# Optimization experiments

Measured on AMD Instinct MI355X. Metric: run time of the kernel, lower is better.

## Reference

```python
import jax, jax.numpy as jnp
from jax import lax
import numpy as np

T_LOW, T_HIGH = 100.0, 200.0  # module defaults
H_IMG, W_IMG = 2048, 2048


def setup_inputs() -> dict:
    key = jax.random.key(0)
    x = jax.random.uniform(key, (H_IMG, W_IMG), dtype=jnp.float32)  # image in [0,1]
    return {"x": x}


def _sh(p, dy, dx, H, W):
    # shifted view of a 1-pixel-padded array
    return p[1 + dy:1 + dy + H, 1 + dx:1 + dx + W]


def _canny(x):
    H, W = x.shape
    # (x*255).astype(uint8): quantize (floor), values assumed in [0,1]
    img = jnp.clip(jnp.floor(x * 255.0), 0.0, 255.0)

    # --- 3x3 Sobel gradients, replicate border (cv2 default) ---
    p = jnp.pad(img, 1, mode='edge')
    s = lambda dy, dx: _sh(p, dy, dx, H, W)
    gx = (s(-1, 1) + 2.0 * s(0, 1) + s(1, 1)) - (s(-1, -1) + 2.0 * s(0, -1) + s(1, -1))
    gy = (s(1, -1) + 2.0 * s(1, 0) + s(1, 1)) - (s(-1, -1) + 2.0 * s(-1, 0) + s(-1, 1))
    mag = jnp.abs(gx) + jnp.abs(gy)  # L1 gradient magnitude (cv2 L2gradient=False)

    # --- non-maximum suppression along quantized gradient direction ---
    ang = jnp.mod(jnp.degrees(jnp.arctan2(gy, gx)), 180.0)
    mp = jnp.pad(mag, 1)  # zero-pad: out-of-image neighbors have magnitude 0
    n = lambda dy, dx: _sh(mp, dy, dx, H, W)
    d0 = (ang < 22.5) | (ang >= 157.5)            # ~0 deg   -> compare L/R
    d1 = (ang >= 22.5) & (ang < 67.5)             # ~45 deg  -> compare diag
    d2 = (ang >= 67.5) & (ang < 112.5)            # ~90 deg  -> compare U/D
    # remaining (~135 deg)                         -> other diag
    n1 = jnp.where(d0, n(0, 1), jnp.where(d1, n(-1, 1), jnp.where(d2, n(-1, 0), n(-1, -1))))
    n2 = jnp.where(d0, n(0, -1), jnp.where(d1, n(1, -1), jnp.where(d2, n(1, 0), n(1, 1))))
    keep = (mag >= n1) & (mag > n2)
    # border pixels are never edges (cv2 behavior)
    interior = jnp.zeros((H, W), bool).at[1:-1, 1:-1].set(True)
    keep = keep & interior

    # --- double threshold + hysteresis edge linking (8-connected) ---
    strong = lax.stop_gradient(keep & (mag > T_HIGH))
    weak = lax.stop_gradient(keep & (mag > T_LOW))

    def dilate8(m):
        mp2 = jnp.pad(m, 1)
        out = jnp.zeros_like(m)
        for dy in (-1, 0, 1):
            for dx in (-1, 0, 1):
                out = out | _sh(mp2, dy, dx, H, W)
        return out

    def body(c):
        cur, _ = c
        new = cur | (weak & dilate8(cur))
        return new, jnp.any(new != cur)

    edges, _ = lax.while_loop(lambda c: c[1], body, (strong, jnp.array(True)))

    # ToTensor() maps uint8 255 -> 1.0; expand to 3 channels
    e = edges.astype(jnp.float32)
    return jnp.broadcast_to(e[None], (3, H, W))


def reference(x):
    return _canny(x)
```

## Files before the change

### kernel.cpp

```cpp
#include <hip/hip_runtime.h>
#include <hip/hip_cooperative_groups.h>

namespace cg = cooperative_groups;

#define HH 2048
#define WW 2048
#define WPR 32
#define NPIX (HH * WW)
#define NWORDS (HH * WPR)

typedef unsigned long long u64;
typedef unsigned int u32;

__device__ inline int findRoot(int* __restrict__ f, int i) {
    int p = __hip_atomic_load(&f[i], __ATOMIC_RELAXED, __HIP_MEMORY_SCOPE_AGENT);
    while (p != i) {
        int gp = __hip_atomic_load(&f[p], __ATOMIC_RELAXED, __HIP_MEMORY_SCOPE_AGENT);
        if (gp != p)
            __hip_atomic_store(&f[i], gp, __ATOMIC_RELAXED, __HIP_MEMORY_SCOPE_AGENT);
        i = p; p = gp;
    }
    return i;
}

__device__ inline void unite(int* __restrict__ f, int a, int b) {
    int ra = findRoot(f, a), rb = findRoot(f, b);
    while (ra != rb) {
        if (ra > rb) { int t = ra; ra = rb; rb = t; }
        int old = atomicCAS(&f[rb], rb, ra);
        if (old == rb || old == ra) return;
        rb = findRoot(f, old);
    }
}

__device__ inline int findRootRO(const int* __restrict__ f, int i) {
    int p = __hip_atomic_load(&f[i], __ATOMIC_RELAXED, __HIP_MEMORY_SCOPE_AGENT);
    while (true) {
        int gp = __hip_atomic_load(&f[p], __ATOMIC_RELAXED, __HIP_MEMORY_SCOPE_AGENT);
        if (gp == p) return p;
        p = gp;
    }
}

__device__ inline int findRootL(volatile int* fl, int i) {
    int p = fl[i];
    while (p != i) {
        int gp = fl[p];
        if (gp != p) fl[i] = gp;
        i = p; p = gp;
    }
    return i;
}

__device__ inline void uniteL(int* fl, int a, int b) {
    int ra = findRootL(fl, a), rb = findRootL(fl, b);
    while (ra != rb) {
        if (ra > rb) { int t = ra; ra = rb; rb = t; }
        int old = atomicCAS(&fl[rb], rb, ra);
        if (old == rb || old == ra) return;
        rb = findRootL(fl, old);
    }
}

__device__ inline int dirClass(int gxv, int gyv) {
    int ay = gyv, ax = gxv;
    if (ay < 0) { ay = -ay; ax = -ax; }
    if (ay == 0) return 0;
    if (ax > 0) {
        int s = ay + ax, q = 2 * ax * ax;
        if (s * s < q) return 0;
        int t = ay - ax;
        return (t < 0 || t * t < q) ? 1 : 2;
    }
    if (ax == 0) return 2;
    int h = -ax, s = ay + h, q = 2 * h * h;
    if (s * s < q) return 0;
    int t = ay - h;
    return (t > 0 && t * t > q) ? 2 : 3;
}

__global__ __launch_bounds__(512) void canny_tile(
    const float* __restrict__ x, u64* __restrict__ weakG,
    u64* __restrict__ strongG, int* __restrict__ f)
{
    __shared__ int imgS[68 * 68];
    __shared__ unsigned short magS[66 * 66];
    __shared__ u64 wRow[64], sRow[64];
    int* fl = imgS;

    const int tid = threadIdx.x;
    const int x0 = blockIdx.x * 64;
    const int y0 = blockIdx.y * 64;

    for (int idx = tid; idx < 68 * 68; idx += 512) {
        int r = idx / 68, c = idx - r * 68;
        int gy = y0 - 2 + r; gy = gy < 0 ? 0 : (gy > HH - 1 ? HH - 1 : gy);
        int gx = x0 - 2 + c; gx = gx < 0 ? 0 : (gx > WW - 1 ? WW - 1 : gx);
        float v = floorf(x[gy * WW + gx] * 255.0f);
        v = fminf(fmaxf(v, 0.0f), 255.0f);
        imgS[idx] = (int)v;
    }
    __syncthreads();

    for (int idx = tid; idx < 66 * 66; idx += 512) {
        int r = idx / 66, c = idx - r * 66;
        int i0 = r * 68 + c;
        int a00 = imgS[i0],       a01 = imgS[i0 + 1],   a02 = imgS[i0 + 2];
        int a10 = imgS[i0 + 68],                        a12 = imgS[i0 + 70];
        int a20 = imgS[i0 + 136], a21 = imgS[i0 + 137], a22 = imgS[i0 + 138];
        int gxv = (a02 + 2 * a12 + a22) - (a00 + 2 * a10 + a20);
        int gyv = (a20 + 2 * a21 + a22) - (a00 + 2 * a01 + a02);
        int mag = abs(gxv) + abs(gyv);
        int cls = dirClass(gxv, gyv);
        magS[idx] = (unsigned short)((cls << 12) | mag);
    }
    __syncthreads();

    const int lane = tid & 63;
    const int wv = tid >> 6;
    for (int i = 0; i < 8; ++i) {
        int rr = wv * 8 + i;
        int gyp = y0 + rr;
        int mc = (rr + 1) * 66 + lane + 1;
        int mv = magS[mc];
        int cls = mv >> 12;
        int mag = mv & 0xFFF;
        int d1 = (cls == 0) ? -1 : 64 + cls;
        int n1 = magS[mc - d1] & 0xFFF;
        int n2 = magS[mc + d1] & 0xFFF;
        bool keep = (mag >= n1) && (mag > n2) && (gyp > 0) && (gyp < HH - 1);
        bool weak = keep && (mag > 100);
        bool strong = keep && (mag > 200);
        u64 ww = __ballot(weak);
        u64 sw = __ballot(strong);
        if (lane == 0) {
            u64 m = ~0ull;
            if (x0 == 0) m &= ~1ull;
            if (x0 + 64 == WW) m &= ~(1ull << 63);
            wRow[rr] = ww & m;
            sRow[rr] = sw & m;
        }
    }
    for (int i = tid; i < 4097; i += 512) fl[i] = i;
    __syncthreads();

    {
        const int r = tid >> 3, o = tid & 7;
        const u64 omask = 0xFFull << (o * 8);
        const u64 w = wRow[r];
        const u64 above = r ? wRow[r - 1] : 0;
        const int base = r * 64 + 1;
        u64 m;
        m = (w & (w >> 1)) & omask;
        while (m) { int b = __builtin_ctzll(m); m &= m - 1; uniteL(fl, base + b, base + b + 1); }
        m = (w & above) & omask;
        while (m) { int b = __builtin_ctzll(m); m &= m - 1; uniteL(fl, base + b, base - 64 + b); }
        m = (w & (above << 1)) & omask;
        while (m) { int b = __builtin_ctzll(m); m &= m - 1; uniteL(fl, base + b, base - 64 + b - 1); }
        m = (w & (above >> 1)) & omask;
        while (m) { int b = __builtin_ctzll(m); m &= m - 1; uniteL(fl, base + b, base - 64 + b + 1); }
        m = sRow[r] & omask;
        while (m) { int b = __builtin_ctzll(m); m &= m - 1; uniteL(fl, 0, base + b); }
    }
    __syncthreads();

    for (int k = 0; k < 8; ++k) {
        int i = k * 512 + tid;
        int rr = i >> 6, cc = i & 63;
        int g = (y0 + rr) * WW + x0 + cc;
        int val = g;
        if ((wRow[rr] >> cc) & 1ull) {
            int rt = findRootL(fl, i + 1);
            val = (rt == 0) ? 0 : (y0 + ((rt - 1) >> 6)) * WW + x0 + ((rt - 1) & 63);
        }
        f[g] = val;
    }
    if (tid < 64) {
        weakG[(y0 + tid) * WPR + blockIdx.x] = wRow[tid];
        strongG[(y0 + tid) * WPR + blockIdx.x] = sRow[tid];
    }
}

__global__ __launch_bounds__(256) void canny_boundary(
    const u64* __restrict__ weakG, int* __restrict__ f)
{
    int t = blockIdx.x * 256 + threadIdx.x;
    if (t < 65536) {
        int y = t >> 5, c = t & 31;
        if (c == 31) return;
        u64 w0 = weakG[y * WPR + c];
        u64 w1 = weakG[y * WPR + c + 1];
        int a = (int)(w0 >> 63) & 1, b = (int)w1 & 1;
        if (!(a | b)) return;
        int p63 = y * WW + c * 64 + 63;
        int p64 = p63 + 1;
        if (a & b) unite(f, p63, p64);
        if (y < HH - 1) {
            u64 w0d = weakG[(y + 1) * WPR + c];
            u64 w1d = weakG[(y + 1) * WPR + c + 1];
            if (a && (w1d & 1ull)) unite(f, p63, p64 + WW);
            if (b && (w0d >> 63)) unite(f, p64, p63 + WW);
        }
    } else {
        int idx = t - 65536;
        if (idx >= 31 * 2048) return;
        int y = 63 + (idx >> 11) * 64;
        int xx = idx & 2047;
        u64 w = weakG[y * WPR + (xx >> 6)];
        if (!((w >> (xx & 63)) & 1ull)) return;
        int p = y * WW + xx;
        u64 wd = weakG[(y + 1) * WPR + (xx >> 6)];
        if ((wd >> (xx & 63)) & 1ull) unite(f, p, p + WW);
        if (xx > 0) {
            u64 wl = weakG[(y + 1) * WPR + ((xx - 1) >> 6)];
            if ((wl >> ((xx - 1) & 63)) & 1ull) unite(f, p, p + WW - 1);
        }
        if (xx < WW - 1) {
            u64 wr = weakG[(y + 1) * WPR + ((xx + 1) >> 6)];
            if ((wr >> ((xx + 1) & 63)) & 1ull) unite(f, p, p + WW + 1);
        }
    }
}

__global__ __launch_bounds__(256) void canny_edgefuse(
    const u64* __restrict__ weakG, const int* __restrict__ f, float* __restrict__ out)
{
    __shared__ unsigned short eS[256];
    const int tid = threadIdx.x;
    const int B = blockIdx.x * 4096;
    const int px0 = B + tid * 16;
    u64 w = weakG[px0 >> 6];
    u32 bits = (u32)(w >> (px0 & 63)) & 0xFFFFu;
    u32 e = 0;
    if (bits) {
        const int4* fq = reinterpret_cast<const int4*>(f + px0);
        int lastp = -1, laste = 0;
        #pragma unroll
        for (int j = 0; j < 4; ++j) {
            int4 q = fq[j];
            #pragma unroll
            for (int k = 0; k < 4; ++k) {
                int b = j * 4 + k;
                if ((bits >> b) & 1u) {
                    int v = (k == 0) ? q.x : (k == 1) ? q.y : (k == 2) ? q.z : q.w;
                    int ed;
                    if (v == 0) ed = 1;
                    else if (v == px0 + b) ed = 0;
                    else if (v == lastp) ed = laste;
                    else { ed = (findRootRO(f, v) == 0); lastp = v; laste = ed; }
                    e |= (u32)ed << b;
                }
            }
        }
    }
    eS[tid] = (unsigned short)e;
    __syncthreads();

    #pragma unroll
    for (int ch = 0; ch < 3; ++ch) {
        #pragma unroll
        for (int j = 0; j < 4; ++j) {
            int idx = j * 256 + tid;
            u32 eb = (u32)(eS[idx >> 2] >> ((idx & 3) * 4)) & 0xFu;
            float4 v;
            v.x = (float)(eb & 1u);
            v.y = (float)((eb >> 1) & 1u);
            v.z = (float)((eb >> 2) & 1u);
            v.w = (float)((eb >> 3) & 1u);
            *reinterpret_cast<float4*>(out + (size_t)ch * NPIX + B + idx * 4) = v;
        }
    }
}

__global__ __launch_bounds__(256) void canny_prep(
    const float* __restrict__ x, u64* __restrict__ weakG,
    u64* __restrict__ strongG, unsigned int* __restrict__ flags)
{
    __shared__ int imgS[20][68];
    __shared__ int magS[18][68];
    const int tid = threadIdx.x;
    const int tx0 = blockIdx.x * 64;
    const int ty0 = blockIdx.y * 16;

    if (flags && blockIdx.x == 0 && blockIdx.y == 0 && tid < 2) flags[tid] = 0u;

    for (int idx = tid; idx < 20 * 68; idx += 256) {
        int r = idx / 68, c = idx - r * 68;
        int gy = ty0 - 2 + r; gy = gy < 0 ? 0 : (gy > HH - 1 ? HH - 1 : gy);
        int gx = tx0 - 2 + c; gx = gx < 0 ? 0 : (gx > WW - 1 ? WW - 1 : gx);
        float v = floorf(x[gy * WW + gx] * 255.0f);
        v = fminf(fmaxf(v, 0.0f), 255.0f);
        imgS[r][c] = (int)v;
    }
    __syncthreads();

    for (int idx = tid; idx < 18 * 66; idx += 256) {
        int r = idx / 66, c = idx - r * 66;
        int a00 = imgS[r][c],     a01 = imgS[r][c + 1],     a02 = imgS[r][c + 2];
        int a10 = imgS[r + 1][c],                           a12 = imgS[r + 1][c + 2];
        int a20 = imgS[r + 2][c], a21 = imgS[r + 2][c + 1], a22 = imgS[r + 2][c + 2];
        int gxv = (a02 + 2 * a12 + a22) - (a00 + 2 * a10 + a20);
        int gyv = (a20 + 2 * a21 + a22) - (a00 + 2 * a01 + a02);
        magS[r][c] = abs(gxv) + abs(gyv);
    }
    __syncthreads();

    const int lane = tid & 63;
    const int wv = tid >> 6;
    for (int i = 0; i < 4; ++i) {
        int rr = wv * 4 + i;
        int gyp = ty0 + rr;
        int r = rr + 1, c = lane + 1;
        int a00 = imgS[rr + 1][lane + 1], a01 = imgS[rr + 1][lane + 2], a02 = imgS[rr + 1][lane + 3];
        int a10 = imgS[rr + 2][lane + 1],                               a12 = imgS[rr + 2][lane + 3];
        int a20 = imgS[rr + 3][lane + 1], a21 = imgS[rr + 3][lane + 2], a22 = imgS[rr + 3][lane + 3];
        int gxv = (a02 + 2 * a12 + a22) - (a00 + 2 * a10 + a20);
        int gyv = (a20 + 2 * a21 + a22) - (a00 + 2 * a01 + a02);
        int mag = magS[r][c];
        int cls = dirClass(gxv, gyv);
        int n1, n2;
        if (cls == 0)      { n1 = magS[r][c + 1];     n2 = magS[r][c - 1]; }
        else if (cls == 1) { n1 = magS[r - 1][c + 1]; n2 = magS[r + 1][c - 1]; }
        else if (cls == 2) { n1 = magS[r - 1][c];     n2 = magS[r + 1][c]; }
        else               { n1 = magS[r - 1][c - 1]; n2 = magS[r + 1][c + 1]; }

        bool keep = (mag >= n1) && (mag > n2) && (gyp > 0) && (gyp < HH - 1);
        bool weak = keep && (mag > 100);
        bool strong = keep && (mag > 200);
        u64 ww = __ballot(weak);
        u64 sw = __ballot(strong);
        if (lane == 0) {
            u64 mm = ~0ull;
            if (tx0 == 0) mm &= ~1ull;
            if (tx0 + 64 == WW) mm &= ~(1ull << 63);
            int widx = gyp * WPR + (tx0 >> 6);
            weakG[widx] = ww & mm;
            strongG[widx] = sw & mm;
        }
    }
}

__global__ __launch_bounds__(256) void canny_hyst(
    const u64* __restrict__ weakG, u64* __restrict__ edgeG,
    unsigned int* __restrict__ flags, float* __restrict__ out)
{
    cg::grid_group grid = cg::this_grid();
    const int tid = threadIdx.x;
    const int b = blockIdx.x;
    const int r = tid >> 5;
    const int c = tid & 31;
    const int row0 = b * 8;
    __shared__ u64 weakL[8][32];
    __shared__ u64 edgeL[10][32];
    __shared__ int sChg[2];
    __shared__ int sAny;

    weakL[r][c] = weakG[(row0 + r) * WPR + c];
    edgeL[r + 1][c] = edgeG[(row0 + r) * WPR + c];

    int iter = 0;
    for (;;) {
        if (tid < 32) {
            u64 v = 0;
            if (b > 0) v = __hip_atomic_load(&edgeG[(row0 - 1) * WPR + tid],
                                             __ATOMIC_RELAXED, __HIP_MEMORY_SCOPE_AGENT);
            edgeL[0][tid] = v;
        } else if (tid < 64) {
            int cc = tid - 32;
            u64 v = 0;
            if (b < (int)gridDim.x - 1)
                v = __hip_atomic_load(&edgeG[(row0 + 8) * WPR + cc],
                                      __ATOMIC_RELAXED, __HIP_MEMORY_SCOPE_AGENT);
            edgeL[9][cc] = v;
        }
        if (tid == 0) sAny = 0;
        if (tid < 2) sChg[tid] = 0;
        __syncthreads();

        int p = 0;
        for (;;) {
            u64 up = edgeL[r][c],     upl = c ? edgeL[r][c - 1] : 0,     upr = (c < 31) ? edgeL[r][c + 1] : 0;
            u64 mi = edgeL[r + 1][c], mil = c ? edgeL[r + 1][c - 1] : 0, mir = (c < 31) ? edgeL[r + 1][c + 1] : 0;
            u64 dn = edgeL[r + 2][c], dnl = c ? edgeL[r + 2][c - 1] : 0, dnr = (c < 31) ? edgeL[r + 2][c + 1] : 0;
            u64 A = up | (up << 1) | (up >> 1) | (upl >> 63) | (upr << 63);
            u64 B = mi | (mi << 1) | (mi >> 1) | (mil >> 63) | (mir << 63);
            u64 C = dn | (dn << 1) | (dn >> 1) | (dnl >> 63) | (dnr << 63);
            u64 ne = mi | (weakL[r][c] & (A | B | C));
            bool chg = (ne != mi);
            __syncthreads();
            edgeL[r + 1][c] = ne;
            if (chg) { sChg[p] = 1; sAny = 1; }
            if (tid == 0) sChg[p ^ 1] = 0;
            __syncthreads();
            if (!sChg[p]) break;
            p ^= 1;
        }

        if (sAny) edgeG[(row0 + r) * WPR + c] = edgeL[r + 1][c];
        if (sAny && tid == 0) atomicOr(&flags[iter & 1], 1u);
        __threadfence();
        grid.sync();
        unsigned fl2 = __hip_atomic_load(&flags[iter & 1], __ATOMIC_ACQUIRE, __HIP_MEMORY_SCOPE_AGENT);
        if (tid == 0) flags[(iter + 1) & 1] = 0u;
        __threadfence();
        grid.sync();
        if (fl2 == 0) break;
        ++iter;
    }

    for (int chn = 0; chn < 3; ++chn) {
        for (int rr = 0; rr < 8; ++rr) {
            size_t base2 = ((size_t)chn * HH + (size_t)(row0 + rr)) * WW;
            for (int k = tid; k < 512; k += 256) {
                u64 w = edgeL[rr + 1][k >> 4];
                int sh = (k & 15) * 4;
                float4 v;
                v.x = (float)((w >> sh) & 1ull);
                v.y = (float)((w >> (sh + 1)) & 1ull);
                v.z = (float)((w >> (sh + 2)) & 1ull);
                v.w = (float)((w >> (sh + 3)) & 1ull);
                *reinterpret_cast<float4*>(out + base2 + (size_t)k * 4) = v;
            }
        }
    }
}

extern "C" void kernel_launch(void* const* d_in, const int* in_sizes, int n_in,
                              void* d_out, int out_size, void* d_ws, size_t ws_size,
                              hipStream_t stream) {
    const float* x = (const float*)d_in[0];
    float* out = (float*)d_out;

    const size_t BM = (size_t)NWORDS * 8;
    const size_t need = 2 * BM + (size_t)NPIX * 4;

    if (ws_size >= need) {
        u64* weakG   = (u64*)d_ws;
        u64* strongG = weakG + NWORDS;
        int* f = (int*)(strongG + NWORDS);

        hipLaunchKernelGGL(canny_tile, dim3(32, 32), dim3(512), 0, stream,
                           x, weakG, strongG, f);
        hipLaunchKernelGGL(canny_boundary, dim3((65536 + 31 * 2048 + 255) / 256), dim3(256),
                           0, stream, weakG, f);
        hipLaunchKernelGGL(canny_edgefuse, dim3(NPIX / 4096), dim3(256), 0, stream,
                           weakG, f, out);
    } else {
        u64* edgeG = (u64*)d_ws;
        u64* weakG = edgeG + NWORDS;
        unsigned int* flags = (unsigned int*)(weakG + NWORDS);
        hipLaunchKernelGGL(canny_prep, dim3(WW / 64, HH / 16), dim3(256), 0, stream,
                           x, weakG, edgeG, flags);
        void* args[] = { (void*)&weakG, (void*)&edgeG, (void*)&flags, (void*)&out };
        hipLaunchCooperativeKernel((void*)canny_hyst, dim3(256), dim3(256), args, 0, stream);
    }
}
```

Measured before the change: 125.8 us.

## Classify tile-local components so edgefuse only resolves border-touching ones

```diff
diff --git a/kernel.cpp b/kernel.cpp
--- a/kernel.cpp
+++ b/kernel.cpp
@@ -81,11 +81,12 @@
 
 __global__ __launch_bounds__(512) void canny_tile(
     const float* __restrict__ x, u64* __restrict__ weakG,
-    u64* __restrict__ strongG, int* __restrict__ f)
+    u64* __restrict__ edgeBits, u64* __restrict__ pendBits, int* __restrict__ f)
 {
     __shared__ int imgS[68 * 68];
     __shared__ unsigned short magS[66 * 66];
     __shared__ u64 wRow[64], sRow[64];
+    __shared__ unsigned char touched[4097];
     int* fl = imgS;
 
     const int tid = threadIdx.x;
@@ -141,7 +142,7 @@
             sRow[rr] = sw & m;
         }
     }
-    for (int i = tid; i < 4097; i += 512) fl[i] = i;
+    for (int i = tid; i < 4097; i += 512) { fl[i] = i; touched[i] = 0; }
     __syncthreads();
 
     {
@@ -164,21 +165,42 @@
     }
     __syncthreads();
 
+    if (tid < 256) {
+        int grp = tid >> 6;
+        int ln = tid & 63;
+        int node = -1;
+        if (grp == 0)      { if ((wRow[0]  >> ln) & 1ull) node = ln + 1; }
+        else if (grp == 1) { if ((wRow[63] >> ln) & 1ull) node = 63 * 64 + ln + 1; }
+        else if (grp == 2) { if (wRow[ln] & 1ull)         node = ln * 64 + 1; }
+        else               { if (wRow[ln] >> 63)          node = ln * 64 + 63 + 1; }
+        if (node > 0) touched[findRootL(fl, node)] = 1;
+    }
+    __syncthreads();
+
     for (int k = 0; k < 8; ++k) {
         int i = k * 512 + tid;
         int rr = i >> 6, cc = i & 63;
         int g = (y0 + rr) * WW + x0 + cc;
         int val = g;
+        bool edge = false, pend = false;
         if ((wRow[rr] >> cc) & 1ull) {
             int rt = findRootL(fl, i + 1);
-            val = (rt == 0) ? 0 : (y0 + ((rt - 1) >> 6)) * WW + x0 + ((rt - 1) & 63);
+            if (rt == 0) { edge = true; val = 0; }
+            else {
+                val = (y0 + ((rt - 1) >> 6)) * WW + x0 + ((rt - 1) & 63);
+                pend = touched[rt] != 0;
+            }
         }
         f[g] = val;
-    }
-    if (tid < 64) {
-        weakG[(y0 + tid) * WPR + blockIdx.x] = wRow[tid];
-        strongG[(y0 + tid) * WPR + blockIdx.x] = sRow[tid];
-    }
+        u64 eb = __ballot(edge);
+        u64 pb = __ballot(pend);
+        if (lane == 0) {
+            int widx = (y0 + rr) * WPR + (x0 >> 6);
+            edgeBits[widx] = eb;
+            pendBits[widx] = pb;
+        }
+    }
+    if (tid < 64) weakG[(y0 + tid) * WPR + blockIdx.x] = wRow[tid];
 }
 
 __global__ __launch_bounds__(256) void canny_boundary(
@@ -223,37 +245,32 @@
 }
 
 __global__ __launch_bounds__(256) void canny_edgefuse(
-    const u64* __restrict__ weakG, const int* __restrict__ f, float* __restrict__ out)
+    const u64* __restrict__ edgeBits, const u64* __restrict__ pendBits,
+    const int* __restrict__ f, float* __restrict__ out)
 {
     __shared__ unsigned short eS[256];
     const int tid = threadIdx.x;
     const int B = blockIdx.x * 4096;
     const int px0 = B + tid * 16;
-    u64 w = weakG[px0 >> 6];
-    u32 bits = (u32)(w >> (px0 & 63)) & 0xFFFFu;
-    u32 e = 0;
-    if (bits) {
-        const int4* fq = reinterpret_cast<const int4*>(f + px0);
+    u64 ew = edgeBits[px0 >> 6];
+    u64 pw = pendBits[px0 >> 6];
+    const int sh = px0 & 63;
+    u32 be = (u32)(ew >> sh) & 0xFFFFu;
+    u32 bp = (u32)(pw >> sh) & 0xFFFFu;
+    if (bp) {
         int lastp = -1, laste = 0;
-        #pragma unroll
-        for (int j = 0; j < 4; ++j) {
-            int4 q = fq[j];
-            #pragma unroll
-            for (int k = 0; k < 4; ++k) {
-                int b = j * 4 + k;
-                if ((bits >> b) & 1u) {
-                    int v = (k == 0) ? q.x : (k == 1) ? q.y : (k == 2) ? q.z : q.w;
-                    int ed;
-                    if (v == 0) ed = 1;
-                    else if (v == px0 + b) ed = 0;
-                    else if (v == lastp) ed = laste;
-                    else { ed = (findRootRO(f, v) == 0); lastp = v; laste = ed; }
-                    e |= (u32)ed << b;
-                }
-            }
-        }
-    }
-    eS[tid] = (unsigned short)e;
+        do {
+            int b = __builtin_ctz(bp); bp &= bp - 1;
+            int v = __hip_atomic_load(&f[px0 + b], __ATOMIC_RELAXED, __HIP_MEMORY_SCOPE_AGENT);
+            int ed;
+            if (v == 0) ed = 1;
+            else if (v == px0 + b) ed = 0;
+            else if (v == lastp) ed = laste;
+            else { ed = (findRootRO(f, v) == 0); lastp = v; laste = ed; }
+            be |= (u32)ed << b;
+        } while (bp);
+    }
+    eS[tid] = (unsigned short)be;
     __syncthreads();
 
     #pragma unroll
@@ -432,19 +449,20 @@
     float* out = (float*)d_out;
 
     const size_t BM = (size_t)NWORDS * 8;
-    const size_t need = 2 * BM + (size_t)NPIX * 4;
+    const size_t need = 3 * BM + (size_t)NPIX * 4;
 
     if (ws_size >= need) {
-        u64* weakG   = (u64*)d_ws;
-        u64* strongG = weakG + NWORDS;
-        int* f = (int*)(strongG + NWORDS);
+        u64* weakG    = (u64*)d_ws;
+        u64* edgeBits = weakG + NWORDS;
+        u64* pendBits = edgeBits + NWORDS;
+        int* f = (int*)(pendBits + NWORDS);
 
         hipLaunchKernelGGL(canny_tile, dim3(32, 32), dim3(512), 0, stream,
-                           x, weakG, strongG, f);
+                           x, weakG, edgeBits, pendBits, f);
         hipLaunchKernelGGL(canny_boundary, dim3((65536 + 31 * 2048 + 255) / 256), dim3(256),
                            0, stream, weakG, f);
         hipLaunchKernelGGL(canny_edgefuse, dim3(NPIX / 4096), dim3(256), 0, stream,
-                           weakG, f, out);
+                           edgeBits, pendBits, f, out);
     } else {
         u64* edgeG = (u64*)d_ws;
         u64* weakG = edgeG + NWORDS;
```

After: 123.8 us. No clear change (-1.6%).
